# Kernel optimization log

Hardware: AMD Instinct MI355X
Metric: run time of the kernel (lower is better)

The kernel has to match this reference:

```python
import jax, jax.numpy as jnp
import numpy as np

EPS = 1e-10
UNK = 2  # token id treated as OOV -> copy slot, per original (w == 2 or w >= vocab_size)


def build_sparse_selective(tokens, V):
    """tokens: [T,B] int. Returns [B,T,V+T] float32.
    Row t+1 gets a one-hot 1.0 at column tokens[t] (or 5.0 at column V+t if OOV/unk),
    everything else EPS — faithful to get_sparse_selective_input (minus vocab-dependent
    slot words, unreachable for in-range random ids)."""
    T, B = tokens.shape
    res = jnp.full((B, T, V + T), EPS, dtype=jnp.float32)
    w = tokens[:-1]                                   # [T-1, B]
    t_idx = jnp.arange(T - 1)
    is_copy = (w == UNK) | (w >= V)
    col = jnp.where(is_copy, V + t_idx[:, None], w)   # [T-1, B]
    val = jnp.where(is_copy, 5.0, 1.0).astype(jnp.float32)
    b_idx = jnp.arange(B)
    res = res.at[b_idx[None, :], (t_idx + 1)[:, None], col].set(val)
    return res


def setup_inputs() -> dict:
    key = jax.random.key(0)
    ks = jax.random.split(key, 20)
    Th, Tu, B, H, E, V = 512, 128, 8, 512, 512, 32000
    s = 1.0 / np.sqrt(H)
    inp = {
        "history_tokens": jax.random.randint(ks[0], (Th, B), 0, V, dtype=jnp.int32),
        "history_enc_out": jax.random.normal(ks[1], (Th, B, H), jnp.float32),
        "u_enc_out": jax.random.normal(ks[2], (Tu, B, H), jnp.float32),
        "c_t_input": jax.random.randint(ks[3], (1, B), 0, V, dtype=jnp.int32),
        "last_hidden": jax.random.normal(ks[4], (1, B, H), jnp.float32),
        # parameters
        "emb_W": jax.random.normal(ks[5], (V, E), jnp.float32) * 0.02,
        "attn_W": jax.random.normal(ks[6], (H, 2 * H), jnp.float32) * s,
        "attn_b": jnp.zeros((H,), jnp.float32),
        "attn_v": jax.random.normal(ks[7], (H,), jnp.float32) * s,
        "gru_Wih": jax.random.normal(ks[8], (3 * H, E + H), jnp.float32) * s,
        "gru_Whh": jax.random.normal(ks[9], (3 * H, H), jnp.float32) * s,
        "gru_bih": jnp.zeros((3 * H,), jnp.float32),
        "gru_bhh": jnp.zeros((3 * H,), jnp.float32),
        "proj_W": jax.random.normal(ks[10], (V, 2 * H), jnp.float32) * s,
        "proj_b": jnp.zeros((V,), jnp.float32),
        "copy2_W": jax.random.normal(ks[11], (H, H), jnp.float32) * s,
        "copy2_b": jnp.zeros((H,), jnp.float32),
        "pgen_W": jax.random.normal(ks[12], (1, 2 * H + E), jnp.float32) * s,
        "pgen_b": jnp.zeros((1,), jnp.float32),
    }
    return inp


def reference(history_tokens, history_enc_out, u_enc_out, c_t_input, last_hidden,
              emb_W, attn_W, attn_b, attn_v, gru_Wih, gru_Whh, gru_bih, gru_bhh,
              proj_W, proj_b, copy2_W, copy2_b, pgen_W, pgen_b):
    V = emb_W.shape[0]
    H = last_hidden.shape[-1]
    h = last_hidden[0]                                    # [B,H]
    c_embed = emb_W[c_t_input[0]]                         # [B,E]

    # --- Attn over u_enc_out ---
    enc = jnp.swapaxes(u_enc_out, 0, 1)                   # [B,Tu,H]
    Hrep = jnp.broadcast_to(h[:, None, :], enc.shape)
    energy = jnp.tanh(jnp.concatenate([Hrep, enc], -1) @ attn_W.T + attn_b)  # [B,Tu,H]
    att = jax.nn.softmax(energy @ attn_v, axis=-1)        # [B,Tu]
    context = jnp.einsum('bt,bth->bh', att, enc)          # [B,H]

    # --- single-step GRU cell (PyTorch semantics) ---
    x = jnp.concatenate([c_embed, context], -1)           # [B,E+H]
    gi = x @ gru_Wih.T + gru_bih
    gh = h @ gru_Whh.T + gru_bhh
    r = jax.nn.sigmoid(gi[:, :H] + gh[:, :H])
    z = jax.nn.sigmoid(gi[:, H:2 * H] + gh[:, H:2 * H])
    n = jnp.tanh(gi[:, 2 * H:] + r * gh[:, 2 * H:])
    h_new = (1.0 - z) * n + z * h                         # gru_out == new hidden (1 layer, 1 step)

    # --- generation score ---
    gen_score = jnp.concatenate([context, h_new], -1) @ proj_W.T + proj_b    # [B,V]

    # --- copy score through sparse selective matrix ---
    sparse = build_sparse_selective(history_tokens, V)    # [B,Th,V+Th]
    hist = jnp.swapaxes(history_enc_out, 0, 1)            # [B,Th,H]
    cs = jnp.tanh(hist @ copy2_W.T + copy2_b)             # [B,Th,H]
    score = jnp.einsum('bth,bh->bt', cs, h_new)           # [B,Th]
    m = jnp.max(score, axis=1, keepdims=True)
    e = jnp.exp(score - m)
    u_copy_score = jnp.log(jnp.einsum('bt,btv->bv', e, sparse)) + m          # [B,V+Th]

    # --- pointer-generator mixing ---
    pgen = jax.nn.sigmoid(jnp.concatenate([context, h_new, c_embed], -1) @ pgen_W.T + pgen_b)  # [B,1]
    scores = jax.nn.softmax(jnp.concatenate([gen_score * pgen, u_copy_score * (1.0 - pgen)], axis=1), axis=1)
    gen, cp = scores[:, :V], scores[:, V:]
    proba = jnp.concatenate([gen + cp[:, :V], cp[:, V:]], axis=1)            # [B,V+Th]
    return proba, h_new[None], h_new[None]
```

## Files before the change

### kernel.cpp

```cpp
#include <hip/hip_runtime.h>
#include <math.h>

#define BB 8
#define TUU 128
#define THH 512
#define HDIM 512
#define VOC 32000
#define WID_ (VOC + THH)

#define OFF_GH      0
#define OFF_BIASATT 12288
#define OFF_CEMB    16384
#define OFF_LATT    20480
#define OFF_SSUM    21504
#define OFF_SCORE   21568
#define OFF_EXTRA   25664
#define OFF_Y       285760
#define OFF_GI      293952
#define OFF_PGEN    306240
#define OFF_M       306248
#define OFF_EPS     306256
#define OFF_WSPLIT_BYTES 1225056

#define OUT_H1 260096
#define OUT_H2 264192

#define SM_SHIFT 20.0f

typedef __attribute__((ext_vector_type(8))) short short8;
typedef __attribute__((ext_vector_type(4))) float f32x4;

__device__ __forceinline__ float wave_sum(float v) {
#pragma unroll
    for (int m = 1; m < 64; m <<= 1) v += __shfl_xor(v, m, 64);
    return v;
}

__device__ __forceinline__ unsigned short f2bf(float x) {
    unsigned int u = __float_as_uint(x);
    unsigned int r = (u + 0x7fffu + ((u >> 16) & 1u)) >> 16;
    return (unsigned short)r;
}
__device__ __forceinline__ float bf2f(unsigned short h) {
    return __uint_as_float(((unsigned int)h) << 16);
}

__global__ __launch_bounds__(256) void k_pre(
    const float* __restrict__ c2W, const float* __restrict__ attn_W,
    const float* __restrict__ attn_b,
    const float* __restrict__ gru_Whh, const float* __restrict__ gru_bhh,
    const float* __restrict__ emb_W, const int* __restrict__ c_t,
    const float* __restrict__ last_h,
    unsigned short* __restrict__ wbase, float* __restrict__ ws)
{
    int bx = blockIdx.x, tid = threadIdx.x;
    if (bx < 1024) {
        int i = bx * 256 + tid;
        float x = c2W[i];
        unsigned short h = f2bf(x);
        wbase[i] = h;
        wbase[262144 + i] = f2bf(x - bf2f(h));
        int j = i >> 9, k = i & 511;
        float y = attn_W[(size_t)j * 1024 + 512 + k];
        unsigned short h2 = f2bf(y);
        wbase[524288 + i] = h2;
        wbase[786432 + i] = f2bf(y - bf2f(h2));
    } else if (bx < 1536) {
        int lane = tid & 63;
        int wid = __builtin_amdgcn_readfirstlane((bx - 1024) * 4 + (tid >> 6));
        const float* wr;
        if (wid < 1536) wr = gru_Whh + (size_t)wid * 512;
        else            wr = attn_W + (size_t)(wid - 1536) * 1024;
        int k = lane * 8;
        float4 w0 = *reinterpret_cast<const float4*>(wr + k);
        float4 w1 = *reinterpret_cast<const float4*>(wr + k + 4);
        float acc[8];
#pragma unroll
        for (int b = 0; b < 8; ++b) {
            const float* hv = last_h + b * 512 + k;
            float4 h0 = *reinterpret_cast<const float4*>(hv);
            float4 h1 = *reinterpret_cast<const float4*>(hv + 4);
            acc[b] = w0.x*h0.x + w0.y*h0.y + w0.z*h0.z + w0.w*h0.w
                   + w1.x*h1.x + w1.y*h1.y + w1.z*h1.z + w1.w*h1.w;
        }
#pragma unroll
        for (int b = 0; b < 8; ++b) acc[b] = wave_sum(acc[b]);
        if (lane == 0) {
            if (wid < 1536) {
                float bias = gru_bhh[wid];
#pragma unroll
                for (int b = 0; b < 8; ++b) ws[OFF_GH + b * 1536 + wid] = acc[b] + bias;
            } else {
                int j = wid - 1536;
                float bias = attn_b[j];
#pragma unroll
                for (int b = 0; b < 8; ++b) ws[OFF_BIASATT + b * 512 + j] = acc[b] + bias;
            }
        }
    } else {
        int idx = (bx - 1536) * 256 + tid;
        int b = idx >> 9, k = idx & 511;
        ws[OFF_CEMB + idx] = emb_W[(size_t)c_t[b] * 512 + k];
    }
}

__device__ __forceinline__ void mfma_tanh_body(
    const float* __restrict__ A,
    const unsigned short* __restrict__ Whi, const unsigned short* __restrict__ Wlo,
    const float* __restrict__ bias, int bstride,
    const float* __restrict__ wvp, int wstride,
    float* __restrict__ outp, int Mout,
    int rbase, int j0,
    short (*As)[64][40], short (*Ws)[128][40])
{
    int tid  = threadIdx.x;
    int lane = tid & 63;
    int wv   = tid >> 6;

    f32x4 acc[4][2];
#pragma unroll
    for (int mt = 0; mt < 4; ++mt)
#pragma unroll
        for (int nt = 0; nt < 2; ++nt) acc[mt][nt] = (f32x4)0.0f;

    int q8  = (lane >> 4) * 8;
    int l15 = lane & 15;
    int ra  = tid >> 2, kk = (tid & 3) * 8;
    int jw  = tid >> 1, kh = (tid & 1) * 16;

    for (int kc = 0; kc < 16; ++kc) {
        int k0 = kc * 32;
        {
            const float* ap = A + (size_t)(rbase + ra) * 512 + k0 + kk;
            float4 a0 = *reinterpret_cast<const float4*>(ap);
            float4 a1 = *reinterpret_cast<const float4*>(ap + 4);
            float vals[8] = {a0.x, a0.y, a0.z, a0.w, a1.x, a1.y, a1.z, a1.w};
            union { short8 v; short s[8]; } hi, lo;
#pragma unroll
            for (int i = 0; i < 8; ++i) {
                unsigned short h = f2bf(vals[i]);
                hi.s[i] = (short)h;
                lo.s[i] = (short)f2bf(vals[i] - bf2f(h));
            }
            *reinterpret_cast<short8*>(&As[0][ra][kk]) = hi.v;
            *reinterpret_cast<short8*>(&As[1][ra][kk]) = lo.v;
        }
        {
            const short8* wph = reinterpret_cast<const short8*>(Whi + (size_t)(j0 + jw) * 512 + k0 + kh);
            const short8* wpl = reinterpret_cast<const short8*>(Wlo + (size_t)(j0 + jw) * 512 + k0 + kh);
            *reinterpret_cast<short8*>(&Ws[0][jw][kh])     = wph[0];
            *reinterpret_cast<short8*>(&Ws[0][jw][kh + 8]) = wph[1];
            *reinterpret_cast<short8*>(&Ws[1][jw][kh])     = wpl[0];
            *reinterpret_cast<short8*>(&Ws[1][jw][kh + 8]) = wpl[1];
        }
        __syncthreads();

        short8 ah[4], al[4], bh[2], bl[2];
#pragma unroll
        for (int mt = 0; mt < 4; ++mt) {
            ah[mt] = *reinterpret_cast<const short8*>(&As[0][mt * 16 + l15][q8]);
            al[mt] = *reinterpret_cast<const short8*>(&As[1][mt * 16 + l15][q8]);
        }
#pragma unroll
        for (int nt = 0; nt < 2; ++nt) {
            bh[nt] = *reinterpret_cast<const short8*>(&Ws[0][wv * 32 + nt * 16 + l15][q8]);
            bl[nt] = *reinterpret_cast<const short8*>(&Ws[1][wv * 32 + nt * 16 + l15][q8]);
        }
#pragma unroll
        for (int mt = 0; mt < 4; ++mt)
#pragma unroll
            for (int nt = 0; nt < 2; ++nt) {
                acc[mt][nt] = __builtin_amdgcn_mfma_f32_16x16x32_bf16(ah[mt], bh[nt], acc[mt][nt], 0, 0, 0);
                acc[mt][nt] = __builtin_amdgcn_mfma_f32_16x16x32_bf16(ah[mt], bl[nt], acc[mt][nt], 0, 0, 0);
                acc[mt][nt] = __builtin_amdgcn_mfma_f32_16x16x32_bf16(al[mt], bh[nt], acc[mt][nt], 0, 0, 0);
            }
        __syncthreads();
    }

    int q = lane >> 4;
#pragma unroll
    for (int mt = 0; mt < 4; ++mt) {
        float s[4];
#pragma unroll
        for (int r = 0; r < 4; ++r) {
            int row = rbase + mt * 16 + q * 4 + r;
            int b = row & 7;
            float v = 0.f;
#pragma unroll
            for (int nt = 0; nt < 2; ++nt) {
                int jj = j0 + wv * 32 + nt * 16 + l15;
                float e = acc[mt][nt][r] + bias[b * bstride + jj];
                v += tanhf(e) * wvp[b * wstride + jj];
            }
#pragma unroll
            for (int m = 1; m < 16; m <<= 1) v += __shfl_xor(v, m, 64);
            s[r] = v;
        }
        if (l15 == 0) {
#pragma unroll
            for (int r = 0; r < 4; ++r) {
                int row = rbase + mt * 16 + q * 4 + r;
                atomicAdd(outp + (row & 7) * Mout + (row >> 3), s[r]);
            }
        }
    }
}

__global__ __launch_bounds__(256) void k_attgemm(
    const float* __restrict__ A, const unsigned short* __restrict__ wsplit,
    const float* __restrict__ attnv, float* __restrict__ ws)
{
    __shared__ short As[2][64][40];
    __shared__ short Ws[2][128][40];
    mfma_tanh_body(A, wsplit + 524288, wsplit + 786432,
                   ws + OFF_BIASATT, 512, attnv, 0,
                   ws + OFF_LATT, 128,
                   blockIdx.x * 64, blockIdx.y * 128, As, Ws);
}

__global__ __launch_bounds__(256) void k_attn_ctx(
    const float* __restrict__ u_enc, float* __restrict__ ws)
{
    __shared__ float red[256];
    __shared__ float att[128];
    int b = blockIdx.x, tid = threadIdx.x;
    float l = (tid < 128) ? ws[OFF_LATT + b * 128 + tid] : -1e30f;
    red[tid] = l; __syncthreads();
    for (int s = 128; s > 0; s >>= 1) {
        if (tid < s) red[tid] = fmaxf(red[tid], red[tid + s]);
        __syncthreads();
    }
    float mm = red[0]; __syncthreads();
    float e = (tid < 128) ? expf(l - mm) : 0.f;
    if (tid < 128) att[tid] = e;
    red[tid] = e; __syncthreads();
    for (int s = 128; s > 0; s >>= 1) {
        if (tid < s) red[tid] += red[tid + s];
        __syncthreads();
    }
    float S = red[0]; __syncthreads();
    float c0 = 0.f, c1 = 0.f;
    for (int t = 0; t < 128; ++t) {
        float a = att[t];
        const float* er = u_enc + (size_t)t * 4096 + b * 512;
        c0 += a * er[tid];
        c1 += a * er[tid + 256];
    }
    float inv = 1.0f / S;
    ws[OFF_Y + b * 1024 + tid]       = c0 * inv;
    ws[OFF_Y + b * 1024 + tid + 256] = c1 * inv;
}

__global__ __launch_bounds__(256) void k_gi(
    const float* __restrict__ gru_Wih, const float* __restrict__ gru_bih,
    float* __restrict__ ws)
{
    int lane = threadIdx.x & 63;
    int r = __builtin_amdgcn_readfirstlane(blockIdx.x * 4 + (threadIdx.x >> 6));
    const float* wr = gru_Wih + (size_t)r * 1024;
    float4 w[4];
#pragma unroll
    for (int p = 0; p < 4; ++p)
        w[p] = *reinterpret_cast<const float4*>(wr + lane * 4 + p * 256);
    float acc[8];
#pragma unroll
    for (int b = 0; b < 8; ++b) {
        acc[b] = 0.f;
#pragma unroll
        for (int p = 0; p < 4; ++p) {
            int k = lane * 4 + p * 256;
            const float* xs = (p < 2) ? (ws + OFF_CEMB + b * 512 + k)
                                      : (ws + OFF_Y + b * 1024 + (k - 512));
            float4 x4 = *reinterpret_cast<const float4*>(xs);
            acc[b] += w[p].x*x4.x + w[p].y*x4.y + w[p].z*x4.z + w[p].w*x4.w;
        }
    }
#pragma unroll
    for (int b = 0; b < 8; ++b) acc[b] = wave_sum(acc[b]);
    if (lane == 0) {
        float bias = gru_bih[r];
#pragma unroll
        for (int b = 0; b < 8; ++b) ws[OFF_GI + b * 1536 + r] = acc[b] + bias;
    }
}

__global__ __launch_bounds__(256) void k_gru(
    const float* __restrict__ last_h,
    const float* __restrict__ pgen_W, const float* __restrict__ pgen_b,
    float* __restrict__ ws, float* __restrict__ out)
{
    __shared__ float red[256];
    int b = blockIdx.x, tid = threadIdx.x;
    const float* gi = ws + OFF_GI + b * 1536;
    const float* gh = ws + OFF_GH + b * 1536;
    float pp = 0.f;
#pragma unroll
    for (int q = 0; q < 2; ++q) {
        int i = tid + q * 256;
        float r = 1.f / (1.f + expf(-(gi[i] + gh[i])));
        float z = 1.f / (1.f + expf(-(gi[512 + i] + gh[512 + i])));
        float n = tanhf(gi[1024 + i] + r * gh[1024 + i]);
        float h = last_h[b * 512 + i];
        float hn = (1.f - z) * n + z * h;
        ws[OFF_Y + b * 1024 + 512 + i] = hn;
        out[OUT_H1 + b * 512 + i] = hn;
        out[OUT_H2 + b * 512 + i] = hn;
        float cx = ws[OFF_Y + b * 1024 + i];
        float ce = ws[OFF_CEMB + b * 512 + i];
        pp += cx * pgen_W[i] + hn * pgen_W[512 + i] + ce * pgen_W[1024 + i];
    }
    red[tid] = pp; __syncthreads();
    for (int s = 128; s > 0; s >>= 1) {
        if (tid < s) red[tid] += red[tid + s];
        __syncthreads();
    }
    if (tid == 0) ws[OFF_PGEN + b] = 1.f / (1.f + expf(-(red[0] + pgen_b[0])));
}

__global__ __launch_bounds__(256) void k_gemmproj(
    const float* __restrict__ henc, const unsigned short* __restrict__ wsplit,
    const float* __restrict__ c2b,
    const float* __restrict__ projW, const float* __restrict__ projb,
    float* __restrict__ ws, float* __restrict__ out)
{
    if (blockIdx.x < 256) {
        __shared__ short As[2][64][40];
        __shared__ short Ws[2][128][40];
        int rbase = (blockIdx.x >> 2) * 64;
        int j0    = (blockIdx.x & 3) * 128;
        mfma_tanh_body(henc, wsplit, wsplit + 262144,
                       c2b, 0, ws + OFF_Y + 512, 1024,
                       ws + OFF_SCORE, 512, rbase, j0, As, Ws);
    } else {
        int lane = threadIdx.x & 63;
        int gw = (blockIdx.x - 256) * 4 + (threadIdx.x >> 6);
        const int nw = 500 * 4;
        float4 yreg[8][4];
#pragma unroll
        for (int b = 0; b < 8; ++b)
#pragma unroll
            for (int p = 0; p < 4; ++p)
                yreg[b][p] = *reinterpret_cast<const float4*>(ws + OFF_Y + b * 1024 + p * 256 + lane * 4);

        for (int v = gw; v < VOC; v += nw) {
            const float4* wr = reinterpret_cast<const float4*>(projW + (size_t)v * 1024);
            float4 w0 = wr[lane], w1 = wr[64 + lane], w2 = wr[128 + lane], w3 = wr[192 + lane];
            float acc[8];
#pragma unroll
            for (int b = 0; b < 8; ++b) {
                acc[b] = w0.x*yreg[b][0].x + w0.y*yreg[b][0].y + w0.z*yreg[b][0].z + w0.w*yreg[b][0].w
                       + w1.x*yreg[b][1].x + w1.y*yreg[b][1].y + w1.z*yreg[b][1].z + w1.w*yreg[b][1].w
                       + w2.x*yreg[b][2].x + w2.y*yreg[b][2].y + w2.z*yreg[b][2].z + w2.w*yreg[b][2].w
                       + w3.x*yreg[b][3].x + w3.y*yreg[b][3].y + w3.z*yreg[b][3].z + w3.w*yreg[b][3].w;
            }
#pragma unroll
            for (int b = 0; b < 8; ++b) acc[b] = wave_sum(acc[b]);
            if (lane == 0) {
                float pb = projb[v];
#pragma unroll
                for (int b = 0; b < 8; ++b) out[b * WID_ + v] = acc[b] + pb;
            }
        }
    }
}

__global__ __launch_bounds__(512) void k_copy_sm(
    const int* __restrict__ htok, float* __restrict__ ws)
{
    __shared__ float red[512];
    __shared__ float es[512];
    int b = blockIdx.x, t = threadIdx.x;
    float s = ws[OFF_SCORE + b * 512 + t];
    red[t] = s; __syncthreads();
    for (int st = 256; st > 0; st >>= 1) {
        if (t < st) red[t] = fmaxf(red[t], red[t + st]);
        __syncthreads();
    }
    float m = red[0]; __syncthreads();
    float e = expf(s - m);
    es[t] = e; red[t] = e; __syncthreads();
    for (int st = 256; st > 0; st >>= 1) {
        if (t < st) red[t] += red[t + st];
        __syncthreads();
    }
    if (t == 0) {
        ws[OFF_M + b]   = m;
        ws[OFF_EPS + b] = 1e-10f * red[0];
    }
    if (t < 511) {
        int tok = htok[t * 8 + b];
        int col = (tok == 2) ? (VOC + t) : tok;
        float val = (tok == 2) ? 5.0f : 1.0f;
        atomicAdd(ws + OFF_EXTRA + b * WID_ + col, (val - 1e-10f) * es[t + 1]);
    }
}

__global__ __launch_bounds__(1024) void k_final2(
    float* __restrict__ ws, float* __restrict__ out)
{
    __shared__ float red[1024];
    int b = blockIdx.x, tid = threadIdx.x;
    float gp   = ws[OFF_PGEN + b];
    float cq   = 1.f - gp;
    float m    = ws[OFF_M + b];
    float epsS = ws[OFF_EPS + b];
    float nums[32];
    float loc = 0.f;
    int cnt = 0;
    for (int w = tid; w < WID_; w += 1024, ++cnt) {
        float ex = ws[OFF_EXTRA + b * WID_ + w];
        float num = expf(cq * (logf(epsS + ex) + m) - SM_SHIFT);
        if (w < VOC) num += expf(gp * out[b * WID_ + w] - SM_SHIFT);
        nums[cnt] = num;
        loc += num;
    }
    red[tid] = loc; __syncthreads();
    for (int st = 512; st > 0; st >>= 1) {
        if (tid < st) red[tid] += red[tid + st];
        __syncthreads();
    }
    float inv = 1.f / red[0];
    cnt = 0;
    for (int w = tid; w < WID_; w += 1024, ++cnt)
        out[b * WID_ + w] = nums[cnt] * inv;
}

extern "C" void kernel_launch(void* const* d_in, const int* in_sizes, int n_in,
                              void* d_out, int out_size, void* d_ws, size_t ws_size,
                              hipStream_t stream)
{
    (void)in_sizes; (void)n_in; (void)out_size; (void)ws_size;
    const int*   htok  = (const int*)d_in[0];
    const float* henc  = (const float*)d_in[1];
    const float* uenc  = (const float*)d_in[2];
    const int*   ct    = (const int*)d_in[3];
    const float* lasth = (const float*)d_in[4];
    const float* embW  = (const float*)d_in[5];
    const float* attnW = (const float*)d_in[6];
    const float* attnb = (const float*)d_in[7];
    const float* attnv = (const float*)d_in[8];
    const float* gWih  = (const float*)d_in[9];
    const float* gWhh  = (const float*)d_in[10];
    const float* gbih  = (const float*)d_in[11];
    const float* gbhh  = (const float*)d_in[12];
    const float* projW = (const float*)d_in[13];
    const float* projb = (const float*)d_in[14];
    const float* c2W   = (const float*)d_in[15];
    const float* c2b   = (const float*)d_in[16];
    const float* pgW   = (const float*)d_in[17];
    const float* pgb   = (const float*)d_in[18];
    float* ws  = (float*)d_ws;
    float* out = (float*)d_out;
    unsigned short* wsplit = (unsigned short*)((char*)d_ws + OFF_WSPLIT_BYTES);

    hipMemsetAsync((char*)d_ws + (size_t)OFF_LATT * 4, 0,
                   (size_t)(OFF_Y - OFF_LATT) * 4, stream);

    k_pre<<<1552, 256, 0, stream>>>(c2W, attnW, attnb, gWhh, gbhh, embW, ct, lasth,
                                    wsplit, ws);
    k_attgemm<<<dim3(16, 4), 256, 0, stream>>>(uenc, wsplit, attnv, ws);
    k_attn_ctx<<<8, 256, 0, stream>>>(uenc, ws);
    k_gi<<<384, 256, 0, stream>>>(gWih, gbih, ws);
    k_gru<<<8, 256, 0, stream>>>(lasth, pgW, pgb, ws, out);
    k_gemmproj<<<756, 256, 0, stream>>>(henc, wsplit, c2b, projW, projb, ws, out);
    k_copy_sm<<<8, 512, 0, stream>>>(htok, ws);
    k_final2<<<8, 1024, 0, stream>>>(ws, out);
}
```

Before: 366.0 us.

## Split fused gemm/proj kernel and parallelize final softmax across blocks

Splits the combined copy-GEMM and vocab projection kernel into two separate launches. The projection gets a 2000-block grid where each wave handles four vocab rows, loaded two at a time for more memory-level parallelism. The final softmax, previously 8 blocks of 1024 threads, becomes a 128-block numerator pass that writes unnormalized values and atomically accumulates per-batch sums, followed by a separate scale pass. This spreads the bandwidth-bound final stage across many CUs, at the cost of an extra launch and an extra read/write of the output. It relies on the OFF_SSUM region being zeroed by the existing memset.

```diff
diff --git a/kernel.cpp b/kernel.cpp
--- a/kernel.cpp
+++ b/kernel.cpp
@@ -218,6 +218,18 @@
                    blockIdx.x * 64, blockIdx.y * 128, As, Ws);
 }
 
+__global__ __launch_bounds__(256) void k_copygemm(
+    const float* __restrict__ A, const unsigned short* __restrict__ wsplit,
+    const float* __restrict__ c2b, float* __restrict__ ws)
+{
+    __shared__ short As[2][64][40];
+    __shared__ short Ws[2][128][40];
+    mfma_tanh_body(A, wsplit, wsplit + 262144,
+                   c2b, 0, ws + OFF_Y + 512, 1024,
+                   ws + OFF_SCORE, 512,
+                   blockIdx.x * 64, blockIdx.y * 128, As, Ws);
+}
+
 __global__ __launch_bounds__(256) void k_attn_ctx(
     const float* __restrict__ u_enc, float* __restrict__ ws)
 {
@@ -317,48 +329,47 @@
     if (tid == 0) ws[OFF_PGEN + b] = 1.f / (1.f + expf(-(red[0] + pgen_b[0])));
 }
 
-__global__ __launch_bounds__(256) void k_gemmproj(
-    const float* __restrict__ henc, const unsigned short* __restrict__ wsplit,
-    const float* __restrict__ c2b,
+__global__ __launch_bounds__(256) void k_proj(
     const float* __restrict__ projW, const float* __restrict__ projb,
-    float* __restrict__ ws, float* __restrict__ out)
-{
-    if (blockIdx.x < 256) {
-        __shared__ short As[2][64][40];
-        __shared__ short Ws[2][128][40];
-        int rbase = (blockIdx.x >> 2) * 64;
-        int j0    = (blockIdx.x & 3) * 128;
-        mfma_tanh_body(henc, wsplit, wsplit + 262144,
-                       c2b, 0, ws + OFF_Y + 512, 1024,
-                       ws + OFF_SCORE, 512, rbase, j0, As, Ws);
-    } else {
-        int lane = threadIdx.x & 63;
-        int gw = (blockIdx.x - 256) * 4 + (threadIdx.x >> 6);
-        const int nw = 500 * 4;
-        float4 yreg[8][4];
-#pragma unroll
-        for (int b = 0; b < 8; ++b)
-#pragma unroll
-            for (int p = 0; p < 4; ++p)
-                yreg[b][p] = *reinterpret_cast<const float4*>(ws + OFF_Y + b * 1024 + p * 256 + lane * 4);
-
-        for (int v = gw; v < VOC; v += nw) {
-            const float4* wr = reinterpret_cast<const float4*>(projW + (size_t)v * 1024);
-            float4 w0 = wr[lane], w1 = wr[64 + lane], w2 = wr[128 + lane], w3 = wr[192 + lane];
-            float acc[8];
+    const float* __restrict__ ws, float* __restrict__ out)
+{
+    int lane = threadIdx.x & 63;
+    int gw = blockIdx.x * 4 + (threadIdx.x >> 6);
+    float4 yreg[8][4];
+#pragma unroll
+    for (int b = 0; b < 8; ++b)
+#pragma unroll
+        for (int p = 0; p < 4; ++p)
+            yreg[b][p] = *reinterpret_cast<const float4*>(ws + OFF_Y + b * 1024 + p * 256 + lane * 4);
+
+    int v0 = gw * 4;
+#pragma unroll
+    for (int pr = 0; pr < 2; ++pr) {
+        int va = v0 + pr * 2;
+        const float4* wra = reinterpret_cast<const float4*>(projW + (size_t)va * 1024);
+        const float4* wrb = reinterpret_cast<const float4*>(projW + (size_t)(va + 1) * 1024);
+        float4 a0 = wra[lane], a1 = wra[64 + lane], a2 = wra[128 + lane], a3 = wra[192 + lane];
+        float4 b0 = wrb[lane], b1 = wrb[64 + lane], b2 = wrb[128 + lane], b3 = wrb[192 + lane];
+        float acca[8], accb[8];
+#pragma unroll
+        for (int b = 0; b < 8; ++b) {
+            acca[b] = a0.x*yreg[b][0].x + a0.y*yreg[b][0].y + a0.z*yreg[b][0].z + a0.w*yreg[b][0].w
+                    + a1.x*yreg[b][1].x + a1.y*yreg[b][1].y + a1.z*yreg[b][1].z + a1.w*yreg[b][1].w
+                    + a2.x*yreg[b][2].x + a2.y*yreg[b][2].y + a2.z*yreg[b][2].z + a2.w*yreg[b][2].w
+                    + a3.x*yreg[b][3].x + a3.y*yreg[b][3].y + a3.z*yreg[b][3].z + a3.w*yreg[b][3].w;
+            accb[b] = b0.x*yreg[b][0].x + b0.y*yreg[b][0].y + b0.z*yreg[b][0].z + b0.w*yreg[b][0].w
+                    + b1.x*yreg[b][1].x + b1.y*yreg[b][1].y + b1.z*yreg[b][1].z + b1.w*yreg[b][1].w
+                    + b2.x*yreg[b][2].x + b2.y*yreg[b][2].y + b2.z*yreg[b][2].z + b2.w*yreg[b][2].w
+                    + b3.x*yreg[b][3].x + b3.y*yreg[b][3].y + b3.z*yreg[b][3].z + b3.w*yreg[b][3].w;
+        }
+#pragma unroll
+        for (int b = 0; b < 8; ++b) { acca[b] = wave_sum(acca[b]); accb[b] = wave_sum(accb[b]); }
+        if (lane == 0) {
+            float pa = projb[va], pb = projb[va + 1];
 #pragma unroll
             for (int b = 0; b < 8; ++b) {
-                acc[b] = w0.x*yreg[b][0].x + w0.y*yreg[b][0].y + w0.z*yreg[b][0].z + w0.w*yreg[b][0].w
-                       + w1.x*yreg[b][1].x + w1.y*yreg[b][1].y + w1.z*yreg[b][1].z + w1.w*yreg[b][1].w
-                       + w2.x*yreg[b][2].x + w2.y*yreg[b][2].y + w2.z*yreg[b][2].z + w2.w*yreg[b][2].w
-                       + w3.x*yreg[b][3].x + w3.y*yreg[b][3].y + w3.z*yreg[b][3].z + w3.w*yreg[b][3].w;
-            }
-#pragma unroll
-            for (int b = 0; b < 8; ++b) acc[b] = wave_sum(acc[b]);
-            if (lane == 0) {
-                float pb = projb[v];
-#pragma unroll
-                for (int b = 0; b < 8; ++b) out[b * WID_ + v] = acc[b] + pb;
+                out[b * WID_ + va]     = acca[b] + pa;
+                out[b * WID_ + va + 1] = accb[b] + pb;
             }
         }
     }
@@ -395,34 +406,41 @@
     }
 }
 
-__global__ __launch_bounds__(1024) void k_final2(
+__global__ __launch_bounds__(256) void k_numer(
     float* __restrict__ ws, float* __restrict__ out)
 {
-    __shared__ float red[1024];
+    __shared__ float red[256];
     int b = blockIdx.x, tid = threadIdx.x;
+    int start = blockIdx.y * 2032;
     float gp   = ws[OFF_PGEN + b];
     float cq   = 1.f - gp;
     float m    = ws[OFF_M + b];
     float epsS = ws[OFF_EPS + b];
-    float nums[32];
     float loc = 0.f;
-    int cnt = 0;
-    for (int w = tid; w < WID_; w += 1024, ++cnt) {
+    for (int w = start + tid; w < start + 2032; w += 256) {
         float ex = ws[OFF_EXTRA + b * WID_ + w];
-        float num = expf(cq * (logf(epsS + ex) + m) - SM_SHIFT);
+        float cv = cq * (logf(epsS + ex) + m);
+        float num = expf(cv - SM_SHIFT);
         if (w < VOC) num += expf(gp * out[b * WID_ + w] - SM_SHIFT);
-        nums[cnt] = num;
+        out[b * WID_ + w] = num;
         loc += num;
     }
     red[tid] = loc; __syncthreads();
-    for (int st = 512; st > 0; st >>= 1) {
+    for (int st = 128; st > 0; st >>= 1) {
         if (tid < st) red[tid] += red[tid + st];
         __syncthreads();
     }
-    float inv = 1.f / red[0];
-    cnt = 0;
-    for (int w = tid; w < WID_; w += 1024, ++cnt)
-        out[b * WID_ + w] = nums[cnt] * inv;
+    if (tid == 0) atomicAdd(ws + OFF_SSUM + b, red[0]);
+}
+
+__global__ __launch_bounds__(256) void k_scale(
+    const float* __restrict__ ws, float* __restrict__ out)
+{
+    int b = blockIdx.x, tid = threadIdx.x;
+    int start = blockIdx.y * 2032;
+    float inv = 1.f / ws[OFF_SSUM + b];
+    for (int w = start + tid; w < start + 2032; w += 256)
+        out[b * WID_ + w] *= inv;
 }
 
 extern "C" void kernel_launch(void* const* d_in, const int* in_sizes, int n_in,
@@ -462,7 +480,9 @@
     k_attn_ctx<<<8, 256, 0, stream>>>(uenc, ws);
     k_gi<<<384, 256, 0, stream>>>(gWih, gbih, ws);
     k_gru<<<8, 256, 0, stream>>>(lasth, pgW, pgb, ws, out);
-    k_gemmproj<<<756, 256, 0, stream>>>(henc, wsplit, c2b, projW, projb, ws, out);
+    k_copygemm<<<dim3(64, 4), 256, 0, stream>>>(henc, wsplit, c2b, ws);
+    k_proj<<<2000, 256, 0, stream>>>(projW, projb, ws, out);
     k_copy_sm<<<8, 512, 0, stream>>>(htok, ws);
-    k_final2<<<8, 1024, 0, stream>>>(ws, out);
-}
+    k_numer<<<dim3(8, 16), 256, 0, stream>>>(ws, out);
+    k_scale<<<dim3(8, 16), 256, 0, stream>>>(ws, out);
+}
```

After: 393.0 us. 7.4% more time.
